# Optimization experiments

Measured on AMD Instinct MI355X. Metric: run time of the kernel, lower is better.

Reference implementation:

```python
import jax, jax.numpy as jnp
import numpy as np

NI = 256        # in_channels
QK = NI // 8    # query/key channels = 32
BS, H, W = 4, 64, 64


def setup_inputs() -> dict:
    key = jax.random.key(0)
    ks = jax.random.split(key, 8)
    x = jax.random.normal(ks[0], (BS, NI, H, W), dtype=jnp.float32)
    # 1x1 conv weights stored as [out_ch, in_ch] (kernel is 1x1)
    wq = jax.random.normal(ks[1], (QK, NI), dtype=jnp.float32) * (1.0 / np.sqrt(NI))
    bq = jnp.zeros((QK,), dtype=jnp.float32)
    wk = jax.random.normal(ks[2], (QK, NI), dtype=jnp.float32) * (1.0 / np.sqrt(NI))
    bk = jnp.zeros((QK,), dtype=jnp.float32)
    wv = jax.random.normal(ks[3], (NI, NI), dtype=jnp.float32) * (1.0 / np.sqrt(NI))
    bv = jnp.zeros((NI,), dtype=jnp.float32)
    # gamma is zero-init in the module; use small random values so the
    # attention branch actually contributes (post-training state).
    gamma = jax.random.normal(ks[4], (1, NI, 1, 1), dtype=jnp.float32) * 0.1
    return {"x": x, "wq": wq, "bq": bq, "wk": wk, "bk": bk,
            "wv": wv, "bv": bv, "gamma": gamma}


def reference(x, wq, bq, wk, bk, wv, bv, gamma):
    bs, c, h, w = x.shape
    n = h * w
    xf = x.reshape(bs, c, n)                       # [bs, c, N]
    # 1x1 convs == per-pixel linear maps over channels
    q = jnp.einsum('oc,bcn->bno', wq, xf) + bq     # [bs, N, qk]
    k = jnp.einsum('oc,bcn->bon', wk, xf) + bk[None, :, None]  # [bs, qk, N]
    v = jnp.einsum('oc,bcn->bon', wv, xf) + bv[None, :, None]  # [bs, c, N]
    attn = jax.nn.softmax(jnp.einsum('bnq,bqm->bnm', q, k), axis=-1)  # [bs, N, N]
    out = jnp.einsum('bcm,bnm->bcn', v, attn)      # value @ attn^T
    out = out.reshape(bs, c, h, w)
    return gamma * out + x
```

## Files before the change

### kernel.cpp

```cpp
#include <hip/hip_runtime.h>
#include <cstdint>
#include <cstddef>

#define NI   256
#define QKC  32
#define BS   4
#define NPIX 4096
#define LOG2E 1.4426950408889634f

typedef __bf16 bf16x8 __attribute__((ext_vector_type(8)));
typedef __bf16 bf16x4 __attribute__((ext_vector_type(4)));
typedef float  f32x16 __attribute__((ext_vector_type(16)));

__device__ inline f32x16 zero16() {
    f32x16 z;
    #pragma unroll
    for (int i = 0; i < 16; ++i) z[i] = 0.f;
    return z;
}

__global__ __launch_bounds__(256) void wconv_pack(
    const float* __restrict__ wq, const float* __restrict__ wk,
    const float* __restrict__ wv, __bf16* __restrict__ wpk)
{
    int f = blockIdx.x * 256 + threadIdx.x;
    int otl = f >> 10, rem = f & 1023;
    int kk = rem >> 6, h = (rem >> 5) & 1, l31 = rem & 31;
    int och = otl * 32 + l31, c0 = kk * 16 + 8 * h;
    const float* src = och < 32 ? wq + och * NI + c0
                     : och < 64 ? wk + (och - 32) * NI + c0
                                : wv + (och - 64) * NI + c0;
    float4 x0 = *(const float4*)src;
    float4 x1 = *(const float4*)(src + 4);
    __align__(16) __bf16 o8[8] = {
        (__bf16)x0.x, (__bf16)x0.y, (__bf16)x0.z, (__bf16)x0.w,
        (__bf16)x1.x, (__bf16)x1.y, (__bf16)x1.z, (__bf16)x1.w};
    *(uint4*)(wpk + (size_t)f * 8) = *(const uint4*)o8;
}

__global__ __launch_bounds__(256) void qkv_mfma(
    const float* __restrict__ x, const __bf16* __restrict__ wpk,
    const float* __restrict__ bq, const float* __restrict__ bk,
    const float* __restrict__ bv,
    __bf16* __restrict__ qpk, __bf16* __restrict__ kpk, __bf16* __restrict__ vpk)
{
    __shared__ __align__(16) __bf16 xT[32][264];
    __shared__ float bls[320];

    const int t = threadIdx.x, w = t >> 6, lane = t & 63;
    const int l31 = lane & 31, h = lane >> 5;
    const int b = blockIdx.y, n0 = blockIdx.x * 32, kt = blockIdx.x;

    for (int i = t; i < 320; i += 256)
        bls[i] = i < 32 ? bq[i] : i < 64 ? bk[i - 32] : bv[i - 64];

    {
        int n4 = (t & 7) * 4, cb = (t >> 3) * 8;
        float4 xv[8];
        #pragma unroll
        for (int j = 0; j < 8; ++j)
            xv[j] = *(const float4*)(x + ((size_t)(b * NI) + cb + j) * NPIX + n0 + n4);
        #pragma unroll
        for (int i = 0; i < 4; ++i) {
            __align__(16) __bf16 r8[8];
            #pragma unroll
            for (int j = 0; j < 8; ++j) r8[j] = (__bf16)((&xv[j].x)[i]);
            *(uint4*)&xT[n4 + i][cb] = *(const uint4*)r8;
        }
    }
    __syncthreads();

    f32x16 acc[3] = {zero16(), zero16(), zero16()};
    #pragma unroll 4
    for (int kk = 0; kk < 16; ++kk) {
        bf16x8 xf = *(const bf16x8*)&xT[l31][kk * 16 + 8 * h];
        #pragma unroll
        for (int jj = 0; jj < 3; ++jj) {
            int otl = w + 4 * jj;
            if (otl < 10) {
                bf16x8 wf = *(const bf16x8*)(wpk + (size_t)((otl * 16 + kk) * 64 + 32 * h + l31) * 8);
                acc[jj] = __builtin_amdgcn_mfma_f32_32x32x16_bf16(wf, xf, acc[jj], 0, 0, 0);
            }
        }
    }
    __syncthreads();

    __bf16 (*vT)[264] = xT;
    #pragma unroll
    for (int jj = 0; jj < 3; ++jj) {
        int otl = w + 4 * jj;
        if (otl >= 2 && otl < 10) {
            #pragma unroll
            for (int qd = 0; qd < 4; ++qd) {
                int c0v = (otl - 2) * 32 + 8 * qd + 4 * h;
                __align__(8) __bf16 q4[4];
                #pragma unroll
                for (int i = 0; i < 4; ++i)
                    q4[i] = (__bf16)(acc[jj][4 * qd + i] + bls[64 + c0v + i]);
                *(uint2*)&vT[l31][c0v] = *(const uint2*)q4;
            }
        }
    }
    #pragma unroll
    for (int jj = 0; jj < 3; ++jj) {
        int otl = w + 4 * jj;
        if (otl == 0) {
            #pragma unroll
            for (int kc = 0; kc < 2; ++kc) {
                __align__(16) __bf16 hi8[8], lo8[8];
                #pragma unroll
                for (int j = 0; j < 8; ++j) {
                    int r = 8 * kc + j;
                    int och = (r & 3) + 8 * (r >> 2) + 4 * h;
                    float val = (acc[jj][r] + bls[och]) * LOG2E;
                    __bf16 hh = (__bf16)val;
                    hi8[j] = hh;
                    lo8[j] = (__bf16)(val - (float)hh);
                }
                size_t base = ((((size_t)(b * 128 + kt) * 2 + 0) * 2 + kc) * 2 + h) * 32 + l31;
                *(uint4*)(qpk + base * 8) = *(const uint4*)hi8;
                size_t basel = ((((size_t)(b * 128 + kt) * 2 + 1) * 2 + kc) * 2 + h) * 32 + l31;
                *(uint4*)(qpk + basel * 8) = *(const uint4*)lo8;
            }
        } else if (otl == 1) {
            #pragma unroll
            for (int kc = 0; kc < 2; ++kc) {
                __align__(16) __bf16 k8[8];
                #pragma unroll
                for (int j = 0; j < 8; ++j) {
                    int r = 8 * kc + j;
                    int och = (r & 3) + 8 * (r >> 2) + 4 * h;
                    k8[j] = (__bf16)(acc[jj][r] + bls[32 + och]);
                }
                size_t base = (((size_t)(b * 128 + kt) * 2 + kc) * 2 + h) * 32 + l31;
                *(uint4*)(kpk + base * 8) = *(const uint4*)k8;
            }
        }
    }
    __syncthreads();

    #pragma unroll
    for (int kc = 0; kc < 2; ++kc)
        #pragma unroll
        for (int hh = 0; hh < 2; ++hh) {
            __align__(16) __bf16 f8[8];
            #pragma unroll
            for (int j = 0; j < 8; ++j) f8[j] = vT[16 * kc + 8 * hh + j][t];
            size_t base = (((size_t)(b * 128 + kt) * 2 + kc) * 2 + hh) * 256 + t;
            *(uint4*)(vpk + base * 8) = *(const uint4*)f8;
        }
}

__global__ __launch_bounds__(512, 4) void attn_mfma(
    const __bf16* __restrict__ qpk, const __bf16* __restrict__ kpk,
    const __bf16* __restrict__ vpk,
    __bf16* __restrict__ Opart, float* __restrict__ dpart)
{
    __shared__ __align__(16) __bf16 pt_s[4][64 * 64];
    __shared__ float dwave[8][32];

    const int t = threadIdx.x;
    const int b = blockIdx.x & 3, ksp = blockIdx.x >> 2;
    const int n0 = blockIdx.y * 64;
    const int w = t >> 6, lane = t & 63, l31 = lane & 31, h = lane >> 5;
    const int q = w & 3, sr = q & 1, sc = q >> 1, pp = w >> 2;
    const int kt0 = ksp * 64;

    const int qt = 2 * blockIdx.y + sr;
    bf16x8 qf[2][2];
    #pragma unroll
    for (int hl = 0; hl < 2; ++hl)
        #pragma unroll
        for (int kc = 0; kc < 2; ++kc)
            qf[hl][kc] = *(const bf16x8*)(qpk +
                (((((size_t)(b * 128 + qt) * 2 + hl) * 2 + kc) * 2 + h) * 32 + l31) * 8);

    auto kload = [&](int ktile, int kc) {
        return *(const bf16x8*)(kpk +
            ((((size_t)(b * 128 + ktile) * 2 + kc) * 2 + h) * 32 + l31) * 8);
    };
    auto vload = [&](int ktile, int kc) {
        return *(const bf16x8*)(vpk +
            ((((size_t)(b * 128 + ktile) * 2 + kc) * 2 + h) * 256 + 32 * w + l31) * 8);
    };

    f32x16 a0 = zero16(), a1 = zero16();
    float dacc = 0.f;

    auto sblock = [&](bf16x8 kh0, bf16x8 kh1, int buf) {
        f32x16 s = zero16();
        __builtin_amdgcn_s_setprio(1);
        s = __builtin_amdgcn_mfma_f32_32x32x16_bf16(kh0, qf[0][0], s, 0, 0, 0);
        s = __builtin_amdgcn_mfma_f32_32x32x16_bf16(kh1, qf[0][1], s, 0, 0, 0);
        s = __builtin_amdgcn_mfma_f32_32x32x16_bf16(kh0, qf[1][0], s, 0, 0, 0);
        s = __builtin_amdgcn_mfma_f32_32x32x16_bf16(kh1, qf[1][1], s, 0, 0, 0);
        __builtin_amdgcn_s_setprio(0);
        char* base = (char*)&pt_s[buf][0];
        const int row = 32 * sr + l31;
        #pragma unroll
        for (int qd = 0; qd < 4; ++qd) {
            __align__(8) __bf16 e4[4];
            #pragma unroll
            for (int i = 0; i < 4; ++i) {
                float e = __builtin_amdgcn_exp2f(s[4 * qd + i]);
                dacc += e;
                e4[i] = (__bf16)e;
            }
            int off = (64 * sc + 16 * qd + 8 * h) ^ ((row & 7) << 4);
            *(uint2*)(base + row * 128 + off) = *(const uint2*)e4;
        }
    };

    auto paread = [&](int buf, int nr, int i, int kc) {
        const int row = 32 * nr + l31;
        int off = (64 * i + 32 * kc + 16 * h) ^ ((row & 7) << 4);
        return *(const bf16x8*)((const char*)&pt_s[buf][0] + row * 128 + off);
    };

    auto pvblock = [&](int m) {
        const int buf = m & 3;
        __builtin_amdgcn_s_setprio(1);
        #pragma unroll
        for (int i = 0; i < 2; ++i)
            #pragma unroll
            for (int kc = 0; kc < 2; ++kc) {
                bf16x8 vfik = vload(kt0 + 2 * m + i, kc);
                bf16x8 pa0 = paread(buf, 0, i, kc);
                bf16x8 pa1 = paread(buf, 1, i, kc);
                a0 = __builtin_amdgcn_mfma_f32_32x32x16_bf16(pa0, vfik, a0, 0, 0, 0);
                a1 = __builtin_amdgcn_mfma_f32_32x32x16_bf16(pa1, vfik, a1, 0, 0, 0);
            }
        __builtin_amdgcn_s_setprio(0);
    };

    bf16x8 kh0 = kload(kt0 + 2 * pp + sc, 0), kh1 = kload(kt0 + 2 * pp + sc, 1);
    sblock(kh0, kh1, pp);
    kh0 = kload(kt0 + 2 * (2 + pp) + sc, 0);
    kh1 = kload(kt0 + 2 * (2 + pp) + sc, 1);
    __syncthreads();

    for (int j = 0; j < 16; ++j) {
        if (j < 15) {
            bf16x8 k0 = kh0, k1 = kh1;
            if (j < 14) {
                const int mtsn = 2 * j + 4 + pp;
                kh0 = kload(kt0 + 2 * mtsn + sc, 0);
                kh1 = kload(kt0 + 2 * mtsn + sc, 1);
            }
            sblock(k0, k1, (2 * j + 2 + pp) & 3);
        }
        pvblock(2 * j);
        pvblock(2 * j + 1);
        __syncthreads();
    }

    float dtot = dacc + __shfl_xor(dacc, 32);
    if (lane < 32) dwave[w][l31] = dtot;
    __syncthreads();
    if (w < 2 && lane < 32) {
        float dsum = dwave[w][l31] + dwave[w + 2][l31]
                   + dwave[w + 4][l31] + dwave[w + 6][l31];
        dpart[((size_t)(ksp * BS + b)) * NPIX + n0 + 32 * w + l31] = dsum;
    }

    size_t obase = (((size_t)(ksp * BS + b)) * NI + 32 * w + l31) * NPIX + n0;
    #pragma unroll
    for (int rq = 0; rq < 4; ++rq) {
        int nn = 8 * rq + 4 * h;
        __align__(8) __bf16 t0[4], t1[4];
        #pragma unroll
        for (int i = 0; i < 4; ++i) {
            t0[i] = (__bf16)a0[4 * rq + i];
            t1[i] = (__bf16)a1[4 * rq + i];
        }
        *(uint2*)(Opart + obase + nn)      = *(const uint2*)t0;
        *(uint2*)(Opart + obase + 32 + nn) = *(const uint2*)t1;
    }
}

__global__ __launch_bounds__(256) void combine(
    const float* __restrict__ x, const float* __restrict__ gamma,
    const __bf16* __restrict__ Opart, const float* __restrict__ dpart,
    float* __restrict__ out)
{
    int idx = (blockIdx.x * 256 + threadIdx.x) * 4;
    int n = idx & (NPIX - 1);
    int c = (idx >> 12) & (NI - 1);
    int b = idx >> 20;

    size_t o0 = (((size_t)(0 * BS + b)) * NI + c) * NPIX + n;
    size_t o1 = (((size_t)(1 * BS + b)) * NI + c) * NPIX + n;
    bf16x4 p0 = *(const bf16x4*)(Opart + o0);
    bf16x4 p1 = *(const bf16x4*)(Opart + o1);
    float4 da = *(const float4*)(dpart + ((size_t)(0 * BS + b)) * NPIX + n);
    float4 db = *(const float4*)(dpart + ((size_t)(1 * BS + b)) * NPIX + n);
    size_t xb = ((size_t)(b * NI) + c) * NPIX + n;
    float4 xv = *(const float4*)(x + xb);
    float g = gamma[c];

    float4 r;
    r.x = g * (((float)p0[0] + (float)p1[0]) / (da.x + db.x)) + xv.x;
    r.y = g * (((float)p0[1] + (float)p1[1]) / (da.y + db.y)) + xv.y;
    r.z = g * (((float)p0[2] + (float)p1[2]) / (da.z + db.z)) + xv.z;
    r.w = g * (((float)p0[3] + (float)p1[3]) / (da.w + db.w)) + xv.w;
    *(float4*)(out + xb) = r;
}

extern "C" void kernel_launch(void* const* d_in, const int* in_sizes, int n_in,
                              void* d_out, int out_size, void* d_ws, size_t ws_size,
                              hipStream_t stream)
{
    const float* x     = (const float*)d_in[0];
    const float* wq    = (const float*)d_in[1];
    const float* bq    = (const float*)d_in[2];
    const float* wk    = (const float*)d_in[3];
    const float* bk    = (const float*)d_in[4];
    const float* wv    = (const float*)d_in[5];
    const float* bv    = (const float*)d_in[6];
    const float* gamma = (const float*)d_in[7];
    float* out = (float*)d_out;

    const size_t WPK = (size_t)10240 * 8;
    const size_t QPK = (size_t)BS * 128 * 2 * 2 * 2 * 32 * 8;
    const size_t KPK = (size_t)BS * 128 * 2 * 2 * 32 * 8;
    const size_t VPK = (size_t)BS * 128 * 2 * 2 * 256 * 8;
    const size_t OSZ = (size_t)2 * BS * NI * NPIX;
    __bf16* wpk   = (__bf16*)d_ws;
    __bf16* qpk   = wpk + WPK;
    __bf16* kpk   = qpk + QPK;
    __bf16* vpk   = kpk + KPK;
    __bf16* Opart = vpk + VPK;
    float*  dpart = (float*)(Opart + OSZ);

    wconv_pack<<<dim3(40), 256, 0, stream>>>(wq, wk, wv, wpk);
    qkv_mfma<<<dim3(NPIX / 32, BS), 256, 0, stream>>>(x, wpk, bq, bk, bv, qpk, kpk, vpk);
    attn_mfma<<<dim3(8, 64), 512, 0, stream>>>(qpk, kpk, vpk, Opart, dpart);
    combine<<<dim3(BS * NI * NPIX / 1024), 256, 0, stream>>>(x, gamma, Opart, dpart, out);
}
```

Before: 157.9 us.

## Repack K/V for contiguous loads and exchange P fragments via shuffles

Changes the packed K and V layouts so that each lane's K fragments and its four V fragments for a tile pair sit contiguously, letting them be fetched with wider, coalesced loads. The softmax probability tile is now rearranged in registers with cross-half lane shuffles and stored in an MFMA-fragment layout in LDS, replacing the swizzled row layout. This cuts the address arithmetic and bank-conflict handling on the LDS reads. The loop is also reordered so the score MFMAs, V prefetch, K prefetch and exp stage interleave, hiding memory latency. The cost is extra shuffle instructions and higher register pressure from holding the prefetched V fragments.

```diff
diff --git a/kernel.cpp b/kernel.cpp
--- a/kernel.cpp
+++ b/kernel.cpp
@@ -132,7 +132,7 @@
                     int och = (r & 3) + 8 * (r >> 2) + 4 * h;
                     k8[j] = (__bf16)(acc[jj][r] + bls[32 + och]);
                 }
-                size_t base = (((size_t)(b * 128 + kt) * 2 + kc) * 2 + h) * 32 + l31;
+                size_t base = (((size_t)(b * 128 + kt) * 2 + h) * 32 + l31) * 2 + kc;
                 *(uint4*)(kpk + base * 8) = *(const uint4*)k8;
             }
         }
@@ -146,7 +146,8 @@
             __align__(16) __bf16 f8[8];
             #pragma unroll
             for (int j = 0; j < 8; ++j) f8[j] = vT[16 * kc + 8 * hh + j][t];
-            size_t base = (((size_t)(b * 128 + kt) * 2 + kc) * 2 + hh) * 256 + t;
+            size_t base = (((((size_t)(b * 64 + (kt >> 1)) * 2 + hh) * 256 + t) * 2
+                            + (kt & 1)) * 2 + kc);
             *(uint4*)(vpk + base * 8) = *(const uint4*)f8;
         }
 }
@@ -156,7 +157,7 @@
     const __bf16* __restrict__ vpk,
     __bf16* __restrict__ Opart, float* __restrict__ dpart)
 {
-    __shared__ __align__(16) __bf16 pt_s[4][64 * 64];
+    __shared__ __align__(16) __bf16 pt_f[4][2][4][64][8];
     __shared__ float dwave[8][32];
 
     const int t = threadIdx.x;
@@ -175,19 +176,18 @@
             qf[hl][kc] = *(const bf16x8*)(qpk +
                 (((((size_t)(b * 128 + qt) * 2 + hl) * 2 + kc) * 2 + h) * 32 + l31) * 8);
 
+    const size_t kinv = (size_t)b * 131072 + (size_t)h * 512 + (size_t)l31 * 16;
+    const size_t vinv = (size_t)b * 1048576 + (size_t)h * 8192
+                      + (size_t)(32 * w + l31) * 32;
+
     auto kload = [&](int ktile, int kc) {
-        return *(const bf16x8*)(kpk +
-            ((((size_t)(b * 128 + ktile) * 2 + kc) * 2 + h) * 32 + l31) * 8);
-    };
-    auto vload = [&](int ktile, int kc) {
-        return *(const bf16x8*)(vpk +
-            ((((size_t)(b * 128 + ktile) * 2 + kc) * 2 + h) * 256 + 32 * w + l31) * 8);
+        return *(const bf16x8*)(kpk + kinv + (size_t)ktile * 1024 + kc * 8);
     };
 
     f32x16 a0 = zero16(), a1 = zero16();
     float dacc = 0.f;
 
-    auto sblock = [&](bf16x8 kh0, bf16x8 kh1, int buf) {
+    auto smma = [&](bf16x8 kh0, bf16x8 kh1) {
         f32x16 s = zero16();
         __builtin_amdgcn_s_setprio(1);
         s = __builtin_amdgcn_mfma_f32_32x32x16_bf16(kh0, qf[0][0], s, 0, 0, 0);
@@ -195,62 +195,84 @@
         s = __builtin_amdgcn_mfma_f32_32x32x16_bf16(kh0, qf[1][0], s, 0, 0, 0);
         s = __builtin_amdgcn_mfma_f32_32x32x16_bf16(kh1, qf[1][1], s, 0, 0, 0);
         __builtin_amdgcn_s_setprio(0);
-        char* base = (char*)&pt_s[buf][0];
-        const int row = 32 * sr + l31;
-        #pragma unroll
-        for (int qd = 0; qd < 4; ++qd) {
-            __align__(8) __bf16 e4[4];
-            #pragma unroll
-            for (int i = 0; i < 4; ++i) {
-                float e = __builtin_amdgcn_exp2f(s[4 * qd + i]);
-                dacc += e;
-                e4[i] = (__bf16)e;
-            }
-            int off = (64 * sc + 16 * qd + 8 * h) ^ ((row & 7) << 4);
-            *(uint2*)(base + row * 128 + off) = *(const uint2*)e4;
-        }
+        return s;
     };
 
-    auto paread = [&](int buf, int nr, int i, int kc) {
-        const int row = 32 * nr + l31;
-        int off = (64 * i + 32 * kc + 16 * h) ^ ((row & 7) << 4);
-        return *(const bf16x8*)((const char*)&pt_s[buf][0] + row * 128 + off);
+    auto sfin = [&](const f32x16& s, int buf) {
+        unsigned xw[8], xs[8];
+        #pragma unroll
+        for (int i = 0; i < 8; ++i) {
+            float e0 = __builtin_amdgcn_exp2f(s[2 * i]);
+            float e1 = __builtin_amdgcn_exp2f(s[2 * i + 1]);
+            dacc += e0 + e1;
+            __align__(4) __bf16 pr[2] = {(__bf16)e0, (__bf16)e1};
+            xw[i] = *(const unsigned*)pr;
+        }
+        #pragma unroll
+        for (int i = 0; i < 8; ++i) xs[i] = __shfl_xor(xw[i], 32);
+        const bool hi = (h != 0);
+        __align__(16) unsigned f0[4], f1[4];
+        f0[0] = hi ? xs[2] : xw[0];  f0[1] = hi ? xs[3] : xw[1];
+        f0[2] = hi ? xw[2] : xs[0];  f0[3] = hi ? xw[3] : xs[1];
+        f1[0] = hi ? xs[6] : xw[4];  f1[1] = hi ? xs[7] : xw[5];
+        f1[2] = hi ? xw[6] : xs[4];  f1[3] = hi ? xw[7] : xs[5];
+        *(uint4*)&pt_f[buf][sr][2 * sc + 0][lane][0] = *(const uint4*)f0;
+        *(uint4*)&pt_f[buf][sr][2 * sc + 1][lane][0] = *(const uint4*)f1;
     };
 
-    auto pvblock = [&](int m) {
-        const int buf = m & 3;
+    auto pvblock = [&](int mt, const bf16x8 (*vf)[2]) {
+        const int buf = mt & 3;
         __builtin_amdgcn_s_setprio(1);
         #pragma unroll
         for (int i = 0; i < 2; ++i)
             #pragma unroll
             for (int kc = 0; kc < 2; ++kc) {
-                bf16x8 vfik = vload(kt0 + 2 * m + i, kc);
-                bf16x8 pa0 = paread(buf, 0, i, kc);
-                bf16x8 pa1 = paread(buf, 1, i, kc);
-                a0 = __builtin_amdgcn_mfma_f32_32x32x16_bf16(pa0, vfik, a0, 0, 0, 0);
-                a1 = __builtin_amdgcn_mfma_f32_32x32x16_bf16(pa1, vfik, a1, 0, 0, 0);
+                const int s2 = 2 * i + kc;
+                bf16x8 pa0 = *(const bf16x8*)&pt_f[buf][0][s2][lane][0];
+                bf16x8 pa1 = *(const bf16x8*)&pt_f[buf][1][s2][lane][0];
+                a0 = __builtin_amdgcn_mfma_f32_32x32x16_bf16(pa0, vf[i][kc], a0, 0, 0, 0);
+                a1 = __builtin_amdgcn_mfma_f32_32x32x16_bf16(pa1, vf[i][kc], a1, 0, 0, 0);
             }
         __builtin_amdgcn_s_setprio(0);
     };
 
     bf16x8 kh0 = kload(kt0 + 2 * pp + sc, 0), kh1 = kload(kt0 + 2 * pp + sc, 1);
-    sblock(kh0, kh1, pp);
+    {
+        f32x16 s = smma(kh0, kh1);
+        sfin(s, pp);
+    }
     kh0 = kload(kt0 + 2 * (2 + pp) + sc, 0);
     kh1 = kload(kt0 + 2 * (2 + pp) + sc, 1);
     __syncthreads();
 
     for (int j = 0; j < 16; ++j) {
-        if (j < 15) {
-            bf16x8 k0 = kh0, k1 = kh1;
-            if (j < 14) {
-                const int mtsn = 2 * j + 4 + pp;
-                kh0 = kload(kt0 + 2 * mtsn + sc, 0);
-                kh1 = kload(kt0 + 2 * mtsn + sc, 1);
-            }
-            sblock(k0, k1, (2 * j + 2 + pp) & 3);
-        }
-        pvblock(2 * j);
-        pvblock(2 * j + 1);
+        f32x16 s;
+        if (j < 15) s = smma(kh0, kh1);
+
+        const __bf16* va = vpk + vinv + (size_t)(ksp * 32 + 2 * j) * 16384;
+        bf16x8 vfa[2][2];
+        #pragma unroll
+        for (int i = 0; i < 2; ++i)
+            #pragma unroll
+            for (int kc = 0; kc < 2; ++kc)
+                vfa[i][kc] = *(const bf16x8*)(va + i * 16 + kc * 8);
+
+        if (j < 14) {
+            const int mtsn = 2 * j + 4 + pp;
+            kh0 = kload(kt0 + 2 * mtsn + sc, 0);
+            kh1 = kload(kt0 + 2 * mtsn + sc, 1);
+        }
+        if (j < 15) sfin(s, (2 * j + 2 + pp) & 3);
+
+        bf16x8 vfb[2][2];
+        #pragma unroll
+        for (int i = 0; i < 2; ++i)
+            #pragma unroll
+            for (int kc = 0; kc < 2; ++kc)
+                vfb[i][kc] = *(const bf16x8*)(va + 16384 + i * 16 + kc * 8);
+
+        pvblock(2 * j, vfa);
+        pvblock(2 * j + 1, vfb);
         __syncthreads();
     }
 
```

After: 162.0 us. +2.6%, slower.
